# Optimization experiments

Hardware: AMD Instinct MI355X
Metric: run time of the kernel (lower is better)

The kernel has to match this reference:

```python
import jax, jax.numpy as jnp
import numpy as np

B, L, C = 8, 2048, 256
D = C // 8  # qk head dim = 32


def _attn(q, k, v, scale):
    # q:[B,L,D] k:[B,L,D] v:[B,L,Dv] -> [B,L,Dv]
    scores = jnp.einsum('bld,bmd->blm', q, k) / scale
    w = jax.nn.softmax(scores, axis=-1)
    return jnp.einsum('blm,bmd->bld', w, v)


def setup_inputs() -> dict:
    key = jax.random.key(0)
    ks = jax.random.split(key, 16)
    he = lambda k, cin, cout: jax.random.normal(k, (cin, cout), jnp.float32) * np.sqrt(2.0 / cin)
    inp = {'x': jax.random.normal(ks[0], (B, L, C, 2), jnp.float32)}
    # 12 1x1 conv kernels (no bias): Q/K -> C//8, V -> C, for 4 attention blocks
    dims = [D, D, C, D, D, C, D, D, C, D, D, C]
    for i, dout in enumerate(dims):
        inp[f'w{i+1}'] = he(ks[i + 1], C, dout)
    inp['alpha'] = jnp.zeros((1,), jnp.float32)
    inp['gamma'] = jnp.zeros((1,), jnp.float32)
    return inp


def reference(x, w1, w2, w3, w4, w5, w6, w7, w8, w9, w10, w11, w12, alpha, gamma):
    ecg = x[:, :, :, 0]  # [B,L,C]
    pcg = x[:, :, :, 1]
    proj = lambda f, w: jnp.einsum('blc,cd->bld', f, w)  # 1x1 conv, no bias
    scale = jnp.sqrt(jnp.asarray(D, x.dtype))

    # ECG intra-attention
    qkv_ecg_intra = _attn(proj(ecg, w1), proj(ecg, w2), proj(ecg, w3), scale)
    # ECG inter-attention (Q from ECG, K/V from PCG)
    qkv_ecg_inter = _attn(proj(ecg, w4), proj(pcg, w5), proj(pcg, w6), scale)
    ecg_out = qkv_ecg_inter + alpha * qkv_ecg_intra

    # PCG intra-attention
    qkv_pcg_intra = _attn(proj(pcg, w7), proj(pcg, w8), proj(pcg, w9), scale)
    # PCG inter-attention (Q from PCG, K/V from ECG)
    qkv_pcg_inter = _attn(proj(pcg, w10), proj(ecg, w11), proj(ecg, w12), scale)
    pcg_out = qkv_pcg_inter + gamma * qkv_pcg_intra

    return jnp.concatenate([ecg_out, pcg_out], axis=-1)  # [B,L,2C]
```

## Files before the change

kernel.cpp:

```cpp
#include <hip/hip_runtime.h>


typedef __bf16 v8bf __attribute__((ext_vector_type(8)));
typedef float  v16f __attribute__((ext_vector_type(16)));
typedef unsigned int u32;

typedef __attribute__((address_space(1))) const void gvoid;
typedef __attribute__((address_space(3))) void svoid;

#define QSCALE 0.25500526817276613f

union frag_u { u32 d[4]; v8bf v; };
union pk_u { unsigned short s[2]; u32 d; };

static __device__ inline u32 pack_bf16(float x, float y) {
  pk_u u;
  __bf16 a = (__bf16)x, b = (__bf16)y;
  u.s[0] = *(unsigned short*)&a;
  u.s[1] = *(unsigned short*)&b;
  return u.d;
}

__global__ __launch_bounds__(256) void deint_kernel(const float* __restrict__ x,
                                                    __bf16* __restrict__ xe,
                                                    __bf16* __restrict__ xp) {
  const size_t i = (size_t)blockIdx.x * 256 + threadIdx.x;
  const float4* xin = (const float4*)(x + i * 16);
  float4 a = xin[0], b = xin[1], c = xin[2], d = xin[3];
  v8bf ev, pv;
  ev[0]=(__bf16)a.x; ev[1]=(__bf16)a.z; ev[2]=(__bf16)b.x; ev[3]=(__bf16)b.z;
  ev[4]=(__bf16)c.x; ev[5]=(__bf16)c.z; ev[6]=(__bf16)d.x; ev[7]=(__bf16)d.z;
  pv[0]=(__bf16)a.y; pv[1]=(__bf16)a.w; pv[2]=(__bf16)b.y; pv[3]=(__bf16)b.w;
  pv[4]=(__bf16)c.y; pv[5]=(__bf16)c.w; pv[6]=(__bf16)d.y; pv[7]=(__bf16)d.w;
  *(v8bf*)(xe + i * 8) = ev;
  *(v8bf*)(xp + i * 8) = pv;
}

struct ProjArgs {
  const __bf16* xe;
  const __bf16* xp;
  const float* w[12];
  __bf16* q[4];
  __bf16* k[4];
  __bf16* vt[4];
  const float* alpha;
  const float* gamma;
};

__global__ __launch_bounds__(256) void proj_kernel(ProjArgs pa) {
  const int job = blockIdx.x;
  const int rb  = blockIdx.y * 128;
  const int tid = threadIdx.x;
  const int lane = tid & 63, w = tid >> 6;
  const int l31 = lane & 31, lh = lane >> 5;
  const int l7 = lane & 7, l8 = lane >> 3;

  __shared__ __bf16 lds_a[4][128 * 64];
  __shared__ __bf16 lds_b[64][264];
  __shared__ __bf16 lds_t[64][136];

  const float gate = job ? pa.gamma[0] : pa.alpha[0];
  const int nchunks = (gate != 0.0f) ? 10 : 6;

  const __bf16* X = job ? pa.xp : pa.xe;
  const char* agbase = (const char*)(X + (size_t)rb*256) + (size_t)(l7 ^ l8)*16
                     + (size_t)l8*512;

#define STAGE_A(kb)                                                             \
  {                                                                             \
    const char* g = agbase + (size_t)(kb)*128;                                  \
    _Pragma("unroll")                                                           \
    for (int i = 0; i < 4; ++i)                                                 \
      __builtin_amdgcn_global_load_lds(                                         \
          (gvoid*)(g + (size_t)(w*4 + i)*8*512),                                \
          (svoid*)&lds_a[kb][((w*4 + i)*8)*64 + lane*8], 16, 0, 0);             \
  }

  STAGE_A(0) STAGE_A(1) STAGE_A(2) STAGE_A(3)
  __syncthreads();

  const int bb = rb >> 11, ll0 = rb & 2047;

  for (int c = 0; c < nchunks; ++c) {
    int vmode = 0, dout = 32, wc0[2] = {0, 0}, vcol0 = 0;
    float sc = 1.0f;
    const float* wp[2];
    __bf16* dqk[2] = {nullptr, nullptr};
    __bf16* vdst = nullptr;
    if (c == 0) {
      sc = QSCALE;
      wp[0] = pa.w[job ? 6 : 0]; wp[1] = pa.w[job ? 9 : 3];
      dqk[0] = pa.q[job ? 2 : 0]; dqk[1] = pa.q[job ? 3 : 1];
    } else if (c == 1) {
      wp[0] = pa.w[job ? 4 : 1]; wp[1] = pa.w[job ? 7 : 10];
      dqk[0] = pa.k[job ? 1 : 0]; dqk[1] = pa.k[job ? 2 : 3];
    } else {
      vmode = 1; dout = 256;
      const int t = (c - 2) & 3;
      const bool second = (c >= 6);
      const int widx = job ? (second ? 8 : 5) : (second ? 2 : 11);
      const int vbuf = job ? (second ? 2 : 1) : (second ? 0 : 3);
      wp[0] = pa.w[widx]; wp[1] = pa.w[widx];
      wc0[0] = t*64; wc0[1] = t*64 + 32;
      vcol0 = t*64; vdst = pa.vt[vbuf];
    }

    for (int h = 0; h < 2; ++h) {
      const float* wgt = wp[h]; const int c0 = wc0[h];
      for (int i = tid; i < 32*256; i += 256) {
        int n = i & 31, kk = i >> 5;
        lds_b[h*32 + n][kk] = (__bf16)wgt[(size_t)kk*dout + c0 + n];
      }
    }
    __syncthreads();

    v16f acc[2];
#pragma unroll
    for (int n = 0; n < 2; ++n)
#pragma unroll
      for (int i = 0; i < 16; ++i) acc[n][i] = 0.f;

#pragma unroll
    for (int kb = 0; kb < 4; ++kb) {
      const __bf16* ab = &lds_a[kb][0];
#pragma unroll
      for (int kk = 0; kk < 4; ++kk) {
        const v8bf af = *(const v8bf*)&ab[(w*32 + l31)*64 + (((kk*2 + lh) ^ (l31 & 7))*8)];
#pragma unroll
        for (int nt = 0; nt < 2; ++nt) {
          const v8bf bf = *(const v8bf*)&lds_b[nt*32 + l31][kb*64 + kk*16 + lh*8];
          acc[nt] = __builtin_amdgcn_mfma_f32_32x32x16_bf16(af, bf, acc[nt], 0, 0, 0);
        }
      }
    }
    __syncthreads();

    if (!vmode) {
#pragma unroll
      for (int nt = 0; nt < 2; ++nt) {
        __bf16* dst = dqk[nt];
#pragma unroll
        for (int r = 0; r < 16; ++r) {
          const int row = rb + w*32 + (r & 3) + 8*(r >> 2) + 4*lh;
          dst[(size_t)row*32 + l31] = (__bf16)(acc[nt][r] * sc);
        }
      }
    } else {
#pragma unroll
      for (int nt = 0; nt < 2; ++nt) {
#pragma unroll
        for (int r = 0; r < 16; ++r) {
          const int row = w*32 + (r & 3) + 8*(r >> 2) + 4*lh;
          lds_t[nt*32 + l31][row] = (__bf16)acc[nt][r];
        }
      }
      __syncthreads();
      const int nt0 = vcol0 >> 5;
      const size_t tbase = (size_t)(bb*32 + (ll0 >> 6));
      for (int i = tid; i < 1024; i += 256) {
        const int ktl = i >> 9, s = i & 511;
        const int h = s >> 8, kc2 = (s >> 5) & 7, v5 = s & 31;
        const int vrow = h*32 + v5, krow = ktl*64 + kc2*8;
        *(int4*)&vdst[((tbase + ktl)*2048 + (size_t)((nt0 + h)*8 + kc2)*32 + v5) * 8] =
            *(const int4*)&lds_t[vrow][krow];
      }
    }
  }
#undef STAGE_A
}

struct FlashArgs {
  const __bf16* q[4];
  const __bf16* k[4];
  const __bf16* v[4];
  const float* alpha;
  const float* gamma;
  float* out;
};

__global__ __launch_bounds__(256, 3) void flash_half(FlashArgs fa) {
  const int flat = blockIdx.x;
  const int pair = flat & 31, qt = flat >> 5;
  const int att = pair & 3, bb = pair >> 2;
  const int tid = threadIdx.x;
  const int lane = tid & 63, w = tid >> 6;
  const int l31 = lane & 31, lh = lane >> 5;

  const float av = fa.alpha[0], gv = fa.gamma[0];
  int att_e, nt0;
  if (att == 0)      { if (av != 0.0f) return; att_e = 1; nt0 = 4; }
  else if (att == 1) { if (av != 0.0f) return; att_e = 1; nt0 = 0; }
  else if (att == 2) { if (gv != 0.0f) return; att_e = 3; nt0 = 4; }
  else               { if (gv != 0.0f) return; att_e = 3; nt0 = 0; }

  __shared__ __bf16 v_lds[2][8192];

  const __bf16* Qp = fa.q[att_e] + (size_t)(bb*2048 + qt*128 + w*32 + l31)*32;
  const __bf16* Kb = fa.k[att_e] + (size_t)bb*2048*32;
  const char* vgbase = (const char*)(fa.v[att_e] + (size_t)bb*32*16384)
                     + (size_t)(nt0*256 + w*256 + lane)*16;
  float* outp = fa.out + (size_t)(bb*2048 + qt*128 + w*32)*512
              + (att_e >> 1)*256 + nt0*32;

  const v8bf qf0 = *(const v8bf*)&Qp[lh*8];
  const v8bf qf1 = *(const v8bf*)&Qp[16 + lh*8];

#define HSTAGE(buf_, kt_)                                                       \
  {                                                                             \
    const char* g = vgbase + (size_t)(kt_)*32768;                               \
    _Pragma("unroll")                                                           \
    for (int i = 0; i < 4; ++i)                                                 \
      __builtin_amdgcn_global_load_lds(                                         \
          (gvoid*)(g + (size_t)i*1024),                                         \
          (svoid*)&v_lds[buf_][(w*256 + 64*i)*8 + lane*8], 16, 0, 0);           \
  }

#define HLOADK(a_, b_, c_, d_, kt_)                                             \
  {                                                                             \
    const int kb_ = (kt_) * 64;                                                 \
    a_ = *(const v8bf*)&Kb[((size_t)(kb_ +      l31))*32 +      lh*8];          \
    b_ = *(const v8bf*)&Kb[((size_t)(kb_ +      l31))*32 + 16 + lh*8];          \
    c_ = *(const v8bf*)&Kb[((size_t)(kb_ + 32 + l31))*32 +      lh*8];          \
    d_ = *(const v8bf*)&Kb[((size_t)(kb_ + 32 + l31))*32 + 16 + lh*8];          \
  }

  v16f acc[4];
#pragma unroll
  for (int n = 0; n < 4; ++n)
#pragma unroll
    for (int i = 0; i < 16; ++i) acc[n][i] = 0.f;
  float den_s = 0.f;

  v8bf kfc00, kfc01, kfc10, kfc11;
  HLOADK(kfc00, kfc01, kfc10, kfc11, 0)
  HSTAGE(0, 0)
  __syncthreads();

#pragma unroll 1
  for (int kt = 0; kt < 32; ++kt) {
    const int cur = kt & 1;
    v8bf kfn00, kfn01, kfn10, kfn11;
    if (kt < 31) {
      HLOADK(kfn00, kfn01, kfn10, kfn11, kt + 1)
      HSTAGE(cur ^ 1, kt + 1)
    }

    v16f st0, st1;
#pragma unroll
    for (int i = 0; i < 16; ++i) { st0[i] = 0.f; st1[i] = 0.f; }
    st0 = __builtin_amdgcn_mfma_f32_32x32x16_bf16(kfc00, qf0, st0, 0, 0, 0);
    st0 = __builtin_amdgcn_mfma_f32_32x32x16_bf16(kfc01, qf1, st0, 0, 0, 0);
    st1 = __builtin_amdgcn_mfma_f32_32x32x16_bf16(kfc10, qf0, st1, 0, 0, 0);
    st1 = __builtin_amdgcn_mfma_f32_32x32x16_bf16(kfc11, qf1, st1, 0, 0, 0);

    u32 pk0[8], pk1[8];
#pragma unroll
    for (int i = 0; i < 8; ++i) {
      const float e0 = __builtin_exp2f(st0[2*i]);
      const float e1 = __builtin_exp2f(st0[2*i + 1]);
      den_s += e0 + e1;
      pk0[i] = pack_bf16(e0, e1);
    }
#pragma unroll
    for (int i = 0; i < 8; ++i) {
      const float e0 = __builtin_exp2f(st1[2*i]);
      const float e1 = __builtin_exp2f(st1[2*i + 1]);
      den_s += e0 + e1;
      pk1[i] = pack_bf16(e0, e1);
    }

    v8bf pf[4];
#pragma unroll
    for (int f2 = 0; f2 < 2; ++f2) {
      u32 a0 = pk0[f2*4 + 0], b0 = pk0[f2*4 + 2];
      u32 a1 = pk0[f2*4 + 1], b1 = pk0[f2*4 + 3];
      asm("v_permlane32_swap_b32 %0, %1" : "+v"(a0), "+v"(b0));
      asm("v_permlane32_swap_b32 %0, %1" : "+v"(a1), "+v"(b1));
      frag_u fu;
      fu.d[0] = a0; fu.d[1] = a1; fu.d[2] = b0; fu.d[3] = b1;
      pf[f2] = fu.v;
    }
#pragma unroll
    for (int f2 = 0; f2 < 2; ++f2) {
      u32 a0 = pk1[f2*4 + 0], b0 = pk1[f2*4 + 2];
      u32 a1 = pk1[f2*4 + 1], b1 = pk1[f2*4 + 3];
      asm("v_permlane32_swap_b32 %0, %1" : "+v"(a0), "+v"(b0));
      asm("v_permlane32_swap_b32 %0, %1" : "+v"(a1), "+v"(b1));
      frag_u fu;
      fu.d[0] = a0; fu.d[1] = a1; fu.d[2] = b0; fu.d[3] = b1;
      pf[2 + f2] = fu.v;
    }

    const __bf16* vb = &v_lds[cur][0];
#pragma unroll
    for (int kc = 0; kc < 4; ++kc)
#pragma unroll
      for (int nt = 0; nt < 4; ++nt) {
        const v8bf vf = *(const v8bf*)&vb[(nt*256 + kc*64 + lane)*8];
        acc[nt] = __builtin_amdgcn_mfma_f32_32x32x16_bf16(pf[kc], vf, acc[nt], 0, 0, 0);
      }

    __syncthreads();
    if (kt < 31) { kfc00 = kfn00; kfc01 = kfn01; kfc10 = kfn10; kfc11 = kfn11; }
  }

  const float den_full = den_s + __shfl_xor(den_s, 32, 64);
#pragma unroll
  for (int r = 0; r < 16; ++r) {
    const int row = (r & 3) + 8*(r >> 2) + 4*lh;
    const float f = 1.0f / __shfl(den_full, row, 64);
#pragma unroll
    for (int nt = 0; nt < 4; ++nt)
      outp[(size_t)row*512 + nt*32 + l31] = acc[nt][r] * f;
  }

#undef HSTAGE
#undef HLOADK
}

template<int NTN>
__device__ __forceinline__ void flash_body(
    const __bf16* __restrict__ Qp, const __bf16* __restrict__ Kb,
    const char* __restrict__ vgbase, float scv, float* __restrict__ outp,
    __bf16* __restrict__ lds0, int lane, int w, int l31, int lh) {

  __bf16* vb0 = lds0;
  __bf16* vb1 = lds0 + NTN*2048;

  const v8bf qf0 = *(const v8bf*)&Qp[lh*8];
  const v8bf qf1 = *(const v8bf*)&Qp[16 + lh*8];

#define STAGE_V(dst_, kt_)                                                      \
  {                                                                             \
    const char* g = vgbase + (size_t)(kt_)*32768;                               \
    _Pragma("unroll")                                                           \
    for (int i = 0; i < NTN; ++i)                                               \
      __builtin_amdgcn_global_load_lds(                                         \
          (gvoid*)(g + (size_t)i*1024),                                         \
          (svoid*)&dst_[(w*NTN*64 + 64*i)*8 + lane*8], 16, 0, 0);               \
  }

  v16f acc[NTN];
#pragma unroll
  for (int n = 0; n < NTN; ++n)
#pragma unroll
    for (int i = 0; i < 16; ++i) acc[n][i] = 0.f;

  float den_s = 0.f;
  v8bf pf[4];
  v8bf kf00, kf01, kf10, kf11;
  v16f st0, st1;
  u32 pk0[8], pk1[8];

#define LOADK(kt_)                                                              \
  {                                                                             \
    const int kb_ = (kt_) * 64;                                                 \
    kf00 = *(const v8bf*)&Kb[((size_t)(kb_ +      l31))*32 +      lh*8];        \
    kf01 = *(const v8bf*)&Kb[((size_t)(kb_ +      l31))*32 + 16 + lh*8];        \
    kf10 = *(const v8bf*)&Kb[((size_t)(kb_ + 32 + l31))*32 +      lh*8];        \
    kf11 = *(const v8bf*)&Kb[((size_t)(kb_ + 32 + l31))*32 + 16 + lh*8];        \
  }

#define SMFMA                                                                   \
  {                                                                             \
    _Pragma("unroll")                                                           \
    for (int i = 0; i < 16; ++i) { st0[i] = 0.f; st1[i] = 0.f; }                \
    st0 = __builtin_amdgcn_mfma_f32_32x32x16_bf16(kf00, qf0, st0, 0, 0, 0);     \
    st0 = __builtin_amdgcn_mfma_f32_32x32x16_bf16(kf01, qf1, st0, 0, 0, 0);     \
    st1 = __builtin_amdgcn_mfma_f32_32x32x16_bf16(kf10, qf0, st1, 0, 0, 0);     \
    st1 = __builtin_amdgcn_mfma_f32_32x32x16_bf16(kf11, qf1, st1, 0, 0, 0);     \
  }

#define EXPH(st_, pk_)                                                          \
  _Pragma("unroll")                                                             \
  for (int i = 0; i < 8; ++i) {                                                 \
    const float e0 = __builtin_exp2f(st_[2*i]);                                 \
    const float e1 = __builtin_exp2f(st_[2*i + 1]);                             \
    den_s += e0 + e1;                                                           \
    pk_[i] = pack_bf16(e0, e1);                                                 \
  }

#define XCHG(pk_, o_)                                                           \
  _Pragma("unroll")                                                             \
  for (int f2 = 0; f2 < 2; ++f2) {                                              \
    u32 a0 = pk_[f2*4 + 0], b0 = pk_[f2*4 + 2];                                 \
    u32 a1 = pk_[f2*4 + 1], b1 = pk_[f2*4 + 3];                                 \
    asm("v_permlane32_swap_b32 %0, %1" : "+v"(a0), "+v"(b0));                   \
    asm("v_permlane32_swap_b32 %0, %1" : "+v"(a1), "+v"(b1));                   \
    frag_u fu;                                                                  \
    fu.d[0] = a0; fu.d[1] = a1; fu.d[2] = b0; fu.d[3] = b1;                     \
    pf[(o_) + f2] = fu.v;                                                       \
  }

#define PVBLK(kc_, vb_)                                                         \
  _Pragma("unroll")                                                             \
  for (int nt = 0; nt < NTN; ++nt) {                                            \
    const v8bf vf = *(const v8bf*)&vb_[(nt*256 + (kc_)*64 + lane)*8];           \
    acc[nt] = __builtin_amdgcn_mfma_f32_32x32x16_bf16(pf[kc_], vf, acc[nt], 0, 0, 0); \
  }

  LOADK(0)
  STAGE_V(vb0, 0)
  SMFMA
  EXPH(st0, pk0)
  EXPH(st1, pk1)
  XCHG(pk0, 0)
  XCHG(pk1, 2)
  __syncthreads();

  for (int kt = 0; kt < 31; ++kt) {
    const int cur = kt & 1;
    LOADK(kt + 1)
    if (cur) { STAGE_V(vb0, kt + 1) } else { STAGE_V(vb1, kt + 1) }
    const __bf16* vb = cur ? vb1 : vb0;

    PVBLK(0, vb)
    SMFMA
    PVBLK(1, vb)
    EXPH(st0, pk0)
    PVBLK(2, vb)
    EXPH(st1, pk1)
    XCHG(pk0, 0)
    PVBLK(3, vb)
    XCHG(pk1, 2)

    __syncthreads();
  }

  {
    PVBLK(0, vb1)
    PVBLK(1, vb1)
    PVBLK(2, vb1)
    PVBLK(3, vb1)
  }

  const float den_full = den_s + __shfl_xor(den_s, 32, 64);
#pragma unroll
  for (int r = 0; r < 16; ++r) {
    const int row = (r & 3) + 8*(r >> 2) + 4*lh;
    const float f = scv / __shfl(den_full, row, 64);
#pragma unroll
    for (int nt = 0; nt < NTN; ++nt)
      unsafeAtomicAdd(&outp[(size_t)row*512 + nt*32 + l31], acc[nt][r] * f);
  }

#undef STAGE_V
#undef LOADK
#undef SMFMA
#undef EXPH
#undef XCHG
#undef PVBLK
}

__global__ __launch_bounds__(256, 2) void flash_full(FlashArgs fa) {
  const int flat = blockIdx.x;
  const int pair = flat & 31, qt = flat >> 5;
  const int att = pair & 3, bb = pair >> 2;
  const int tid = threadIdx.x;
  const int lane = tid & 63, w = tid >> 6;
  const int l31 = lane & 31, lh = lane >> 5;

  const float av = fa.alpha[0], gv = fa.gamma[0];
  float scv = 1.0f;
  if (att == 0)      { if (av == 0.0f) return; scv = av; }
  else if (att == 1) { if (av == 0.0f) return; }
  else if (att == 2) { if (gv == 0.0f) return; scv = gv; }
  else               { if (gv == 0.0f) return; }

  __shared__ __bf16 v_lds[2][16384];

  const __bf16* Qp = fa.q[att] + (size_t)(bb*2048 + qt*128 + w*32 + l31)*32;
  const __bf16* Kb = fa.k[att] + (size_t)bb*2048*32;
  const char* vgbase = (const char*)(fa.v[att] + (size_t)bb*32*16384)
                     + (size_t)(w*512 + lane)*16;
  float* outp = fa.out + (size_t)(bb*2048 + qt*128 + w*32)*512 + (att >> 1)*256;

  flash_body<8>(Qp, Kb, vgbase, scv, outp, &v_lds[0][0], lane, w, l31, lh);
}

extern "C" void kernel_launch(void* const* d_in, const int* in_sizes, int n_in,
                              void* d_out, int out_size, void* d_ws, size_t ws_size,
                              hipStream_t stream) {
  (void)in_sizes; (void)n_in; (void)out_size; (void)ws_size;

  __bf16* wsp = (__bf16*)d_ws;
  const size_t XE = (size_t)16384 * 256;
  const size_t QK = (size_t)16384 * 32;
  const size_t VT = (size_t)8 * 32 * 16384;

  __bf16* xe = wsp;
  __bf16* xp = wsp + XE;

  ProjArgs pa;
  pa.xe = xe; pa.xp = xp;
  const float* x = (const float*)d_in[0];
  for (int i = 0; i < 12; ++i) pa.w[i] = (const float*)d_in[1 + i];
  __bf16* base = wsp + 2*XE;
  for (int i = 0; i < 4; ++i) pa.q[i]  = base + (size_t)i * QK;
  for (int i = 0; i < 4; ++i) pa.k[i]  = base + (size_t)(4 + i) * QK;
  for (int i = 0; i < 4; ++i) pa.vt[i] = base + 8*QK + (size_t)i * VT;
  pa.alpha = (const float*)d_in[13];
  pa.gamma = (const float*)d_in[14];

  hipMemsetAsync(d_out, 0, (size_t)8*2048*512*4, stream);
  hipLaunchKernelGGL(deint_kernel, dim3(2048), dim3(256), 0, stream, x, xe, xp);
  hipLaunchKernelGGL(proj_kernel, dim3(2, 128), dim3(256), 0, stream, pa);

  FlashArgs fl;
  for (int i = 0; i < 4; ++i) { fl.q[i] = pa.q[i]; fl.k[i] = pa.k[i]; fl.v[i] = pa.vt[i]; }
  fl.alpha = (const float*)d_in[13];
  fl.gamma = (const float*)d_in[14];
  fl.out = (float*)d_out;
  hipLaunchKernelGGL(flash_half, dim3(512), dim3(256), 0, stream, fl);
  hipLaunchKernelGGL(flash_full, dim3(512), dim3(256), 0, stream, fl);
}
```

Measured before the change: 246.8 us.

## Split projection kernel into per-output-chunk jobs with smaller row tiles

The projection kernel previously ran 2x128 blocks, each looping serially over up to 10 weight chunks for 128 rows. It now launches 10x256 blocks, one per (job, 64-row tile), where each block computes only two chunks and each wave owns one 32x32 output tile. Blocks whose gate (alpha/gamma) is zero exit early. This exposes far more parallelism to fill the GPU, in exchange for reloading the input rows in several blocks and launching many idle blocks when the gates are zero.

Result: faster. 239.2 us (-3.1%).

```diff
diff --git a/kernel.cpp b/kernel.cpp
--- a/kernel.cpp
+++ b/kernel.cpp
@@ -49,20 +49,24 @@
 
 __global__ __launch_bounds__(256) void proj_kernel(ProjArgs pa) {
   const int job = blockIdx.x;
-  const int rb  = blockIdx.y * 128;
+  const int rb  = blockIdx.y * 64;
   const int tid = threadIdx.x;
   const int lane = tid & 63, w = tid >> 6;
+  const int rh = w >> 1, ch = w & 1;
   const int l31 = lane & 31, lh = lane >> 5;
   const int l7 = lane & 7, l8 = lane >> 3;
 
-  __shared__ __bf16 lds_a[4][128 * 64];
+  if (job >= 6) {
+    if (job < 8) { if (pa.alpha[0] == 0.0f) return; }
+    else         { if (pa.gamma[0] == 0.0f) return; }
+  }
+  const int src = (0x332 >> job) & 1;
+
+  __shared__ __bf16 lds_a[4][64 * 64];
   __shared__ __bf16 lds_b[64][264];
-  __shared__ __bf16 lds_t[64][136];
-
-  const float gate = job ? pa.gamma[0] : pa.alpha[0];
-  const int nchunks = (gate != 0.0f) ? 10 : 6;
-
-  const __bf16* X = job ? pa.xp : pa.xe;
+  __shared__ __bf16 lds_t[64][72];
+
+  const __bf16* X = src ? pa.xp : pa.xe;
   const char* agbase = (const char*)(X + (size_t)rb*256) + (size_t)(l7 ^ l8)*16
                      + (size_t)l8*512;
 
@@ -70,36 +74,38 @@
   {                                                                             \
     const char* g = agbase + (size_t)(kb)*128;                                  \
     _Pragma("unroll")                                                           \
-    for (int i = 0; i < 4; ++i)                                                 \
+    for (int i = 0; i < 2; ++i)                                                 \
       __builtin_amdgcn_global_load_lds(                                         \
-          (gvoid*)(g + (size_t)(w*4 + i)*8*512),                                \
-          (svoid*)&lds_a[kb][((w*4 + i)*8)*64 + lane*8], 16, 0, 0);             \
+          (gvoid*)(g + (size_t)(w*2 + i)*8*512),                                \
+          (svoid*)&lds_a[kb][((w*2 + i)*8)*64 + lane*8], 16, 0, 0);             \
   }
 
   STAGE_A(0) STAGE_A(1) STAGE_A(2) STAGE_A(3)
   __syncthreads();
 
-  const int bb = rb >> 11, ll0 = rb & 2047;
-
-  for (int c = 0; c < nchunks; ++c) {
+  const int bb = rb >> 11, ktl = (rb & 2047) >> 6;
+
+  for (int c = 0; c < 2; ++c) {
     int vmode = 0, dout = 32, wc0[2] = {0, 0}, vcol0 = 0;
     float sc = 1.0f;
     const float* wp[2];
     __bf16* dqk[2] = {nullptr, nullptr};
     __bf16* vdst = nullptr;
-    if (c == 0) {
-      sc = QSCALE;
-      wp[0] = pa.w[job ? 6 : 0]; wp[1] = pa.w[job ? 9 : 3];
-      dqk[0] = pa.q[job ? 2 : 0]; dqk[1] = pa.q[job ? 3 : 1];
-    } else if (c == 1) {
-      wp[0] = pa.w[job ? 4 : 1]; wp[1] = pa.w[job ? 7 : 10];
-      dqk[0] = pa.k[job ? 1 : 0]; dqk[1] = pa.k[job ? 2 : 3];
+    if (job < 2) {
+      if (c == 0) {
+        sc = QSCALE;
+        wp[0] = pa.w[job ? 6 : 0]; wp[1] = pa.w[job ? 9 : 3];
+        dqk[0] = pa.q[job ? 2 : 0]; dqk[1] = pa.q[job ? 3 : 1];
+      } else {
+        wp[0] = pa.w[job ? 4 : 1]; wp[1] = pa.w[job ? 7 : 10];
+        dqk[0] = pa.k[job ? 1 : 0]; dqk[1] = pa.k[job ? 2 : 3];
+      }
     } else {
       vmode = 1; dout = 256;
-      const int t = (c - 2) & 3;
-      const bool second = (c >= 6);
-      const int widx = job ? (second ? 8 : 5) : (second ? 2 : 11);
-      const int vbuf = job ? (second ? 2 : 1) : (second ? 0 : 3);
+      const int vj = job - 2, vg = vj >> 1;
+      const int t = (vj & 1)*2 + c;
+      const int widx = (vg==0) ? 11 : (vg==1) ? 5 : (vg==2) ? 2 : 8;
+      const int vbuf = (vg==0) ? 3  : (vg==1) ? 1 : (vg==2) ? 0 : 2;
       wp[0] = pa.w[widx]; wp[1] = pa.w[widx];
       wc0[0] = t*64; wc0[1] = t*64 + 32;
       vcol0 = t*64; vdst = pa.vt[vbuf];
@@ -114,55 +120,40 @@
     }
     __syncthreads();
 
-    v16f acc[2];
-#pragma unroll
-    for (int n = 0; n < 2; ++n)
-#pragma unroll
-      for (int i = 0; i < 16; ++i) acc[n][i] = 0.f;
-
+    v16f acc;
+#pragma unroll
+    for (int i = 0; i < 16; ++i) acc[i] = 0.f;
 #pragma unroll
     for (int kb = 0; kb < 4; ++kb) {
       const __bf16* ab = &lds_a[kb][0];
 #pragma unroll
       for (int kk = 0; kk < 4; ++kk) {
-        const v8bf af = *(const v8bf*)&ab[(w*32 + l31)*64 + (((kk*2 + lh) ^ (l31 & 7))*8)];
-#pragma unroll
-        for (int nt = 0; nt < 2; ++nt) {
-          const v8bf bf = *(const v8bf*)&lds_b[nt*32 + l31][kb*64 + kk*16 + lh*8];
-          acc[nt] = __builtin_amdgcn_mfma_f32_32x32x16_bf16(af, bf, acc[nt], 0, 0, 0);
-        }
+        const v8bf af = *(const v8bf*)&ab[(rh*32 + l31)*64 + (((kk*2 + lh) ^ (l31 & 7))*8)];
+        const v8bf bf = *(const v8bf*)&lds_b[ch*32 + l31][kb*64 + kk*16 + lh*8];
+        acc = __builtin_amdgcn_mfma_f32_32x32x16_bf16(af, bf, acc, 0, 0, 0);
       }
     }
     __syncthreads();
 
     if (!vmode) {
-#pragma unroll
-      for (int nt = 0; nt < 2; ++nt) {
-        __bf16* dst = dqk[nt];
-#pragma unroll
-        for (int r = 0; r < 16; ++r) {
-          const int row = rb + w*32 + (r & 3) + 8*(r >> 2) + 4*lh;
-          dst[(size_t)row*32 + l31] = (__bf16)(acc[nt][r] * sc);
-        }
+      __bf16* dst = dqk[ch];
+#pragma unroll
+      for (int r = 0; r < 16; ++r) {
+        const int row = rb + rh*32 + (r & 3) + 8*(r >> 2) + 4*lh;
+        dst[(size_t)row*32 + l31] = (__bf16)(acc[r] * sc);
       }
     } else {
 #pragma unroll
-      for (int nt = 0; nt < 2; ++nt) {
-#pragma unroll
-        for (int r = 0; r < 16; ++r) {
-          const int row = w*32 + (r & 3) + 8*(r >> 2) + 4*lh;
-          lds_t[nt*32 + l31][row] = (__bf16)acc[nt][r];
-        }
+      for (int r = 0; r < 16; ++r) {
+        const int row = rh*32 + (r & 3) + 8*(r >> 2) + 4*lh;
+        lds_t[ch*32 + l31][row] = (__bf16)acc[r];
       }
       __syncthreads();
       const int nt0 = vcol0 >> 5;
-      const size_t tbase = (size_t)(bb*32 + (ll0 >> 6));
-      for (int i = tid; i < 1024; i += 256) {
-        const int ktl = i >> 9, s = i & 511;
-        const int h = s >> 8, kc2 = (s >> 5) & 7, v5 = s & 31;
-        const int vrow = h*32 + v5, krow = ktl*64 + kc2*8;
-        *(int4*)&vdst[((tbase + ktl)*2048 + (size_t)((nt0 + h)*8 + kc2)*32 + v5) * 8] =
-            *(const int4*)&lds_t[vrow][krow];
+      for (int i = tid; i < 512; i += 256) {
+        const int h = i >> 8, kc2 = (i >> 5) & 7, v5 = i & 31;
+        *(int4*)&vdst[((size_t)(bb*32 + ktl)*2048 + (size_t)((nt0 + h)*8 + kc2)*32 + v5) * 8] =
+            *(const int4*)&lds_t[h*32 + v5][kc2*8];
       }
     }
   }
@@ -504,7 +495,7 @@
 
   hipMemsetAsync(d_out, 0, (size_t)8*2048*512*4, stream);
   hipLaunchKernelGGL(deint_kernel, dim3(2048), dim3(256), 0, stream, x, xe, xp);
-  hipLaunchKernelGGL(proj_kernel, dim3(2, 128), dim3(256), 0, stream, pa);
+  hipLaunchKernelGGL(proj_kernel, dim3(10, 256), dim3(256), 0, stream, pa);
 
   FlashArgs fl;
   for (int i = 0; i < 4; ++i) { fl.q[i] = pa.q[i]; fl.k[i] = pa.k[i]; fl.v[i] = pa.vt[i]; }
```
